# Optimization experiments

Measured on AMD Instinct MI355X. Metric: run time of the kernel, lower is better.

The kernel has to match this reference:

```python
import jax, jax.numpy as jnp
import numpy as np
import math

D_MODEL = 768
HEADS = 12
D_FF = 3072
B, S = 2, 2048


def layer_norm(x, g, b, eps=1e-6):
    mu = jnp.mean(x, axis=-1, keepdims=True)
    var = jnp.mean((x - mu) ** 2, axis=-1, keepdims=True)
    return (x - mu) / jnp.sqrt(var + eps) * g + b


def gelu_tanh(x):
    c = math.sqrt(2.0 / math.pi)
    return 0.5 * x * (1.0 + jnp.tanh(c * (x + 0.044715 * x ** 3)))


def setup_inputs() -> dict:
    key = jax.random.key(0)
    ks = jax.random.split(key, 12)
    s = 0.02
    inp = {
        "iter": 1,
        "query": jax.random.normal(ks[0], (B, S, D_MODEL), jnp.float32),
        "inputs": jax.random.normal(ks[1], (B, S, D_MODEL), jnp.float32),
        "mask": jax.random.randint(ks[2], (B, S), 0, 2).astype(bool),
        "Wq": jax.random.normal(ks[3], (D_MODEL, D_MODEL), jnp.float32) * s,
        "bq": jnp.zeros((D_MODEL,), jnp.float32),
        "Wk": jax.random.normal(ks[4], (D_MODEL, D_MODEL), jnp.float32) * s,
        "bk": jnp.zeros((D_MODEL,), jnp.float32),
        "Wv": jax.random.normal(ks[5], (D_MODEL, D_MODEL), jnp.float32) * s,
        "bv": jnp.zeros((D_MODEL,), jnp.float32),
        "Wo": jax.random.normal(ks[6], (D_MODEL, D_MODEL), jnp.float32) * s,
        "bo": jnp.zeros((D_MODEL,), jnp.float32),
        "ln1_g": jnp.ones((D_MODEL,), jnp.float32),
        "ln1_b": jnp.zeros((D_MODEL,), jnp.float32),
        "W1": jax.random.normal(ks[7], (D_MODEL, D_FF), jnp.float32) * s,
        "b1": jnp.zeros((D_FF,), jnp.float32),
        "W2": jax.random.normal(ks[8], (D_FF, D_MODEL), jnp.float32) * s,
        "b2": jnp.zeros((D_MODEL,), jnp.float32),
        "ln2_g": jnp.ones((D_MODEL,), jnp.float32),
        "ln2_b": jnp.zeros((D_MODEL,), jnp.float32),
    }
    return inp


def reference(iter, query, inputs, mask, Wq, bq, Wk, bk, Wv, bv, Wo, bo,
              ln1_g, ln1_b, W1, b1, W2, b2, ln2_g, ln2_b):
    dh = D_MODEL // HEADS
    # pre-LN (skipped when iter == 0)
    x = layer_norm(inputs, ln1_g, ln1_b) if iter != 0 else inputs
    # QKV projections -> [B, H, S, dh]
    def heads(t):
        return t.reshape(B, S, HEADS, dh).transpose(0, 2, 1, 3)
    q = heads(x @ Wq + bq) / math.sqrt(dh)
    k = heads(x @ Wk + bk)
    v = heads(x @ Wv + bv)
    scores = jnp.einsum("bhqd,bhkd->bhqk", q, k)
    scores = jnp.where(mask[:, None, None, :], -1e18, scores)
    attn = jax.nn.softmax(scores, axis=-1)
    ctx = jnp.einsum("bhqk,bhkd->bhqd", attn, v)
    ctx = ctx.transpose(0, 2, 1, 3).reshape(B, S, D_MODEL)
    attn_out = ctx @ Wo + bo
    out = attn_out + inputs  # dropout=0 -> identity
    # FFN with residual pre-LN and tanh-GELU
    h = layer_norm(out, ln2_g, ln2_b)
    inter = gelu_tanh(h @ W1 + b1)
    return inter @ W2 + b2 + out
```

## Files before the change

kernel.cpp:

```cpp
#include <hip/hip_runtime.h>
#include <hip/hip_bf16.h>
#include <stdint.h>

#define D_MODEL 768
#define HEADS   12
#define DHEAD   64
#define D_FF    3072
#define BB      2
#define SS      2048
#define MTOT    (BB*SS)

typedef uint16_t u16;
typedef uint32_t u32;
typedef __attribute__((ext_vector_type(8))) short short8;
typedef __attribute__((ext_vector_type(4))) short short4v;
typedef __attribute__((ext_vector_type(4))) float f32x4;
typedef __attribute__((ext_vector_type(16))) float f32x16;
typedef __attribute__((ext_vector_type(2))) unsigned uint2v;

__device__ __forceinline__ u16 f2bf(float f) {
    union { float f; u32 u; } v; v.f = f;
    u32 r = v.u + 0x7fffu + ((v.u >> 16) & 1u);
    return (u16)(r >> 16);
}

__device__ __forceinline__ float bf2f(u16 u) {
    union { u32 u; float f; } v; v.u = ((u32)u) << 16;
    return v.f;
}

__device__ __forceinline__ float exp2_fast(float x) {
#if __has_builtin(__builtin_amdgcn_exp2f)
    return __builtin_amdgcn_exp2f(x);
#else
    return exp2f(x);
#endif
}

__device__ __forceinline__ u32 cvtpk(float a, float b) {
    u32 r;
    asm("v_cvt_pk_bf16_f32 %0, %1, %2" : "=v"(r) : "v"(a), "v"(b));
    return r;
}

__device__ __forceinline__ void plswap(u32& a, u32& b, int hi) {
#if __has_builtin(__builtin_amdgcn_permlane32_swap)
    uint2v r = __builtin_amdgcn_permlane32_swap(a, b, false, false);
    a = r[0]; b = r[1];
#else
    u32 ax = (u32)__shfl_xor((int)a, 32), bx = (u32)__shfl_xor((int)b, 32);
    u32 na = hi ? bx : a, nb = hi ? b : ax;
    a = na; b = nb;
#endif
}

__device__ __forceinline__ void gload16(const void* g, void* l) {
    __builtin_amdgcn_global_load_lds(
        (const __attribute__((address_space(1))) u32*)g,
        (__attribute__((address_space(3))) u32*)l, 16, 0, 0);
}

#define MFMA16(a, b, c) __builtin_amdgcn_mfma_f32_16x16x32_bf16((a), (b), (c), 0, 0, 0)
#define MFMA32(a, b, c) __builtin_amdgcn_mfma_f32_32x32x16_bf16((a), (b), (c), 0, 0, 0)

__device__ __forceinline__ float gelu_tanh_f(float x) {
    float x3 = x * x * x;
    return 0.5f * x * (1.0f + tanhf(0.7978845608028654f * (x + 0.044715f * x3)));
}

__global__ __launch_bounds__(256)
void transpose_cast(const float* __restrict__ W, u16* __restrict__ Wt, int R, int C) {
    __shared__ float tile[32][33];
    int bx = blockIdx.x, by = blockIdx.y;
    int x = threadIdx.x & 31, y0 = threadIdx.x >> 5;
#pragma unroll
    for (int i = 0; i < 4; ++i) {
        int y = y0 + i * 8;
        tile[y][x] = W[(size_t)(by * 32 + y) * C + bx * 32 + x];
    }
    __syncthreads();
#pragma unroll
    for (int i = 0; i < 4; ++i) {
        int y = y0 + i * 8;
        Wt[(size_t)(bx * 32 + y) * R + by * 32 + x] = f2bf(tile[x][y]);
    }
}

__global__ __launch_bounds__(256)
void transpose_cast4(const float* __restrict__ W0, const float* __restrict__ W1,
                     const float* __restrict__ W2, const float* __restrict__ W3,
                     u16* __restrict__ T0, u16* __restrict__ T1,
                     u16* __restrict__ T2, u16* __restrict__ T3) {
    const int z = blockIdx.z;
    const float* W = z == 0 ? W0 : z == 1 ? W1 : z == 2 ? W2 : W3;
    u16*         T = z == 0 ? T0 : z == 1 ? T1 : z == 2 ? T2 : T3;
    __shared__ float tile[32][33];
    int bx = blockIdx.x, by = blockIdx.y;
    int x = threadIdx.x & 31, y0 = threadIdx.x >> 5;
#pragma unroll
    for (int i = 0; i < 4; ++i) {
        int y = y0 + i * 8;
        tile[y][x] = W[(size_t)(by * 32 + y) * 768 + bx * 32 + x];
    }
    __syncthreads();
#pragma unroll
    for (int i = 0; i < 4; ++i) {
        int y = y0 + i * 8;
        T[(size_t)(bx * 32 + y) * 768 + by * 32 + x] = f2bf(tile[x][y]);
    }
}

__global__ void maskprep(const int* __restrict__ m, float* __restrict__ vz,
                         u16* __restrict__ m01, int n) {
    int i = blockIdx.x * 256 + threadIdx.x;
    if (i < n) {
        float v = m[i] ? 0.0f : 1.0f;
        vz[i] = v;
        m01[i] = f2bf(v);
    }
}

__global__ __launch_bounds__(256)
void ln_bf16(const float* __restrict__ in, const float* __restrict__ g,
             const float* __restrict__ bta, u16* __restrict__ out,
             const int* __restrict__ iterp, int checkIter) {
    int row = blockIdx.x, tid = threadIdx.x;
    const float* x = in + (size_t)row * D_MODEL;
    float v0 = x[tid], v1 = x[tid + 256], v2 = x[tid + 512];
    float s = v0 + v1 + v2;
    float s2 = v0 * v0 + v1 * v1 + v2 * v2;
#pragma unroll
    for (int o = 1; o < 64; o <<= 1) { s += __shfl_xor(s, o); s2 += __shfl_xor(s2, o); }
    __shared__ float sh[8];
    int w = tid >> 6;
    if ((tid & 63) == 0) { sh[w] = s; sh[4 + w] = s2; }
    __syncthreads();
    s = sh[0] + sh[1] + sh[2] + sh[3];
    s2 = sh[4] + sh[5] + sh[6] + sh[7];
    float mu = s * (1.0f / 768.0f);
    float var = s2 * (1.0f / 768.0f) - mu * mu;
    float rstd = rsqrtf(var + 1e-6f);
    bool skip = checkIter && (iterp[0] == 0);
    u16* o0 = out + (size_t)row * D_MODEL;
    if (skip) {
        o0[tid] = f2bf(v0); o0[tid + 256] = f2bf(v1); o0[tid + 512] = f2bf(v2);
    } else {
        o0[tid]       = f2bf((v0 - mu) * rstd * g[tid]       + bta[tid]);
        o0[tid + 256] = f2bf((v1 - mu) * rstd * g[tid + 256] + bta[tid + 256]);
        o0[tid + 512] = f2bf((v2 - mu) * rstd * g[tid + 512] + bta[tid + 512]);
    }
}

__global__ __launch_bounds__(256)
void ln_fuse(const float* __restrict__ pf, const float* __restrict__ bias,
             const float* __restrict__ res, const float* __restrict__ g,
             const float* __restrict__ bta, float* __restrict__ outm,
             u16* __restrict__ out) {
    int row = blockIdx.x, tid = threadIdx.x;
    size_t i0 = (size_t)row * D_MODEL + tid;
    const float* pf1 = pf + (size_t)MTOT * D_MODEL;
    float v0 = pf[i0]       + pf1[i0]       + bias[tid]       + res[i0];
    float v1 = pf[i0 + 256] + pf1[i0 + 256] + bias[tid + 256] + res[i0 + 256];
    float v2 = pf[i0 + 512] + pf1[i0 + 512] + bias[tid + 512] + res[i0 + 512];
    outm[i0] = v0; outm[i0 + 256] = v1; outm[i0 + 512] = v2;
    float s = v0 + v1 + v2;
    float s2 = v0 * v0 + v1 * v1 + v2 * v2;
#pragma unroll
    for (int o = 1; o < 64; o <<= 1) { s += __shfl_xor(s, o); s2 += __shfl_xor(s2, o); }
    __shared__ float sh[8];
    int w = tid >> 6;
    if ((tid & 63) == 0) { sh[w] = s; sh[4 + w] = s2; }
    __syncthreads();
    s = sh[0] + sh[1] + sh[2] + sh[3];
    s2 = sh[4] + sh[5] + sh[6] + sh[7];
    float mu = s * (1.0f / 768.0f);
    float var = s2 * (1.0f / 768.0f) - mu * mu;
    float rstd = rsqrtf(var + 1e-6f);
    u16* o0 = out + (size_t)row * D_MODEL;
    o0[tid]       = f2bf((v0 - mu) * rstd * g[tid]       + bta[tid]);
    o0[tid + 256] = f2bf((v1 - mu) * rstd * g[tid + 256] + bta[tid + 256]);
    o0[tid + 512] = f2bf((v2 - mu) * rstd * g[tid + 512] + bta[tid + 512]);
}

template <int MODE>
__global__ __launch_bounds__(256, 3)
void gemm_bt(const u16* __restrict__ A, const u16* __restrict__ Bt,
             int K, int N,
             const float* __restrict__ bias0, const float* __restrict__ bias1,
             const float* __restrict__ bias2,
             const float* __restrict__ res,
             float* __restrict__ outF, u16* __restrict__ oq,
             u16* __restrict__ ok, u16* __restrict__ ov) {
    __shared__ __align__(16) u16 aT[3][128 * 32];
    __shared__ __align__(16) u16 bT[3][128 * 32];
    const int tid = threadIdx.x;
    const int lane = tid & 63;
    const int w = tid >> 6;
    const int wr = w >> 1, wc = w & 1;
    const int lm = lane & 15, lq = lane >> 4;
    const int bm = blockIdx.y, bn = blockIdx.x;
    const int kzlen = K / gridDim.z;
    const int kbeg = blockIdx.z * kzlen;
    const int nsteps = kzlen >> 5;

    const u16* Abase = A  + (size_t)(bm * 128) * K + kbeg;
    const u16* Bbase = Bt + (size_t)(bn * 128) * K + kbeg;

    auto stage = [&](int buf, int t) {
        int k0 = t * 32;
#pragma unroll
        for (int j = 0; j < 2; ++j) {
            int d = j * 256 + tid;
            int row = d >> 2, p = d & 3;
            int src = (p ^ (row & 3)) * 8;
            gload16(Abase + (size_t)row * K + k0 + src, aT[buf] + (j * 256 + w * 64) * 8);
            gload16(Bbase + (size_t)row * K + k0 + src, bT[buf] + (j * 256 + w * 64) * 8);
        }
    };

    f32x4 acc[4][4] = {};
    stage(0, 0);
    if (nsteps > 1) stage(1, 1);

#pragma unroll 1
    for (int t = 0; t < nsteps; ++t) {
        if (t + 1 < nsteps) asm volatile("s_waitcnt vmcnt(4)" ::: "memory");
        else                asm volatile("s_waitcnt vmcnt(0)" ::: "memory");
        __syncthreads();
        const u16* Ab = aT[t % 3];
        const u16* Bb = bT[t % 3];
        short8 av[4], bv[4];
#pragma unroll
        for (int m = 0; m < 4; ++m) {
            int row = wr * 64 + m * 16 + lm;
            av[m] = *(const short8*)(Ab + row * 32 + ((lq ^ (row & 3)) * 8));
        }
#pragma unroll
        for (int n = 0; n < 4; ++n) {
            int row = wc * 64 + n * 16 + lm;
            bv[n] = *(const short8*)(Bb + row * 32 + ((lq ^ (row & 3)) * 8));
        }
#pragma unroll
        for (int m = 0; m < 4; ++m)
#pragma unroll
            for (int n = 0; n < 4; ++n)
                acc[m][n] = MFMA16(av[m], bv[n], acc[m][n]);
        if (t + 2 < nsteps) stage((t + 2) % 3, t + 2);
    }

#pragma unroll
    for (int m = 0; m < 4; ++m) {
#pragma unroll
        for (int n = 0; n < 4; ++n) {
            int col = bn * 128 + wc * 64 + n * 16 + lm;
#pragma unroll
            for (int r = 0; r < 4; ++r) {
                int row = bm * 128 + wr * 64 + m * 16 + lq * 4 + r;
                float v = acc[m][n][r];
                if (MODE == 0) {
                    int proj = col / D_MODEL;
                    int d = col - proj * D_MODEL;
                    int hh = d >> 6, dhi = d & 63;
                    int bb = row >> 11, sIdx = row & 2047;
                    if (proj == 0) {
                        v = (v + bias0[d]) * 0.18033688011112042f;
                        oq[((size_t)(bb * HEADS + hh) * SS + sIdx) * DHEAD + dhi] = f2bf(v);
                    } else if (proj == 1) {
                        v = v + bias1[d];
                        ok[((size_t)(bb * HEADS + hh) * SS + sIdx) * DHEAD + dhi] = f2bf(v);
                    } else {
                        v = (v + bias2[d]) * res[row];
                        ov[((size_t)(bb * HEADS + hh) * DHEAD + dhi) * SS + sIdx] = f2bf(v);
                    }
                } else if (MODE == 1) {
                    if (gridDim.z > 1) {
                        outF[((size_t)blockIdx.z * MTOT + row) * N + col] = v;
                    } else {
                        size_t idx = (size_t)row * N + col;
                        outF[idx] = v + bias0[col] + res[idx];
                    }
                } else {
                    float t2 = v + bias0[col];
                    oq[(size_t)row * N + col] = f2bf(gelu_tanh_f(t2));
                }
            }
        }
    }
}

__global__ __launch_bounds__(256)
void reduce_ks2(const float* __restrict__ pf, const float* __restrict__ bias,
                const float* __restrict__ res, float* __restrict__ out, int N) {
    size_t i = ((size_t)blockIdx.x * 256 + threadIdx.x) * 4;
    f32x4 s0 = *(const f32x4*)(pf + i);
    f32x4 s1 = *(const f32x4*)(pf + (size_t)MTOT * N + i);
    int col = (int)(i % (size_t)N);
    f32x4 b = *(const f32x4*)(bias + col);
    f32x4 r = *(const f32x4*)(res + i);
    f32x4 o;
#pragma unroll
    for (int e = 0; e < 4; ++e) o[e] = s0[e] + s1[e] + b[e] + r[e];
    *(f32x4*)(out + i) = o;
}

template <int NCH>
__global__ __launch_bounds__(256, 3)
void attn_fwd6(const u16* __restrict__ q, const u16* __restrict__ k,
               const u16* __restrict__ vtg, const u16* __restrict__ m01g,
               u16* __restrict__ po, float* __restrict__ pml) {
    constexpr int KLEN = SS / NCH;
    constexpr int KT   = KLEN / 64;
    __shared__ __align__(16) u16 kls[3][64 * 64];
    __shared__ __align__(16) u16 vls[3][64 * 64];
    __shared__ __align__(16) u16 m01l[KLEN];

    const int tid = threadIdx.x, lane = tid & 63, w = tid >> 6;
    const int lm = lane & 31, hi = lane >> 5;
    const int head = blockIdx.y;
    const int qblk = blockIdx.x / NCH, chunk = blockIdx.x % NCH;
    const int q0 = qblk * 128;
    const int k0 = chunk * KLEN;

    const u16* qbase = q + (size_t)head * SS * DHEAD;
    const u16* kbase = k + (size_t)head * SS * DHEAD;
    const u16* vbase = vtg + (size_t)head * DHEAD * SS;
    const u16* m01row = m01g + (head / HEADS) * SS;

    short8 qf[4];
    const int qrow = q0 + w * 32 + lm;
#pragma unroll
    for (int c = 0; c < 4; ++c)
        qf[c] = *(const short8*)(qbase + (size_t)qrow * DHEAD + c * 16 + hi * 8);

    if (tid < KLEN / 8)
        gload16(m01row + k0 + (size_t)tid * 8, m01l + (size_t)(tid >> 6) * 64 * 8);

    auto stage = [&](int buf, int t) {
#pragma unroll
        for (int j = 0; j < 2; ++j) {
            int c = j * 256 + tid;
            int row = c >> 3, jj = c & 7;
            gload16(kbase + (size_t)(k0 + t * 64 + row) * DHEAD + ((jj ^ (row & 7)) * 8),
                    kls[buf] + (j * 256 + w * 64) * 8);
            gload16(vbase + (size_t)row * SS + k0 + t * 64 + ((jj ^ (row & 7)) * 8),
                    vls[buf] + (j * 256 + w * 64) * 8);
        }
    };
    stage(0, 0);
    if (KT > 1) stage(1, 1);

    f32x16 o0 = {}, o1 = {}, accl = {};

#pragma unroll 1
    for (int t = 0; t < KT; ++t) {
        if (t + 1 < KT) asm volatile("s_waitcnt vmcnt(4)" ::: "memory");
        else            asm volatile("s_waitcnt vmcnt(0)" ::: "memory");
        __syncthreads();
        const u16* kb = kls[t % 3];
        const u16* vb = vls[t % 3];
#pragma unroll
        for (int s = 0; s < 2; ++s) {
            short8 av[4];
#pragma unroll
            for (int c = 0; c < 4; ++c)
                av[c] = *(const short8*)(kb + (s * 32 + lm) * 64 + (((c * 2 + hi) ^ (lm & 7)) * 8));
            short8 vf[4];
#pragma unroll
            for (int kc = 0; kc < 2; ++kc)
#pragma unroll
                for (int df = 0; df < 2; ++df)
                    vf[kc * 2 + df] = *(const short8*)(vb + (df * 32 + lm) * 64 +
                                                       (((s * 4 + kc * 2 + hi) ^ (lm & 7)) * 8));
            short8 mf0 = *(const short8*)(m01l + t * 64 + s * 32 + hi * 8);
            short8 mf1 = *(const short8*)(m01l + t * 64 + s * 32 + 16 + hi * 8);

            f32x16 st = {};
#pragma unroll
            for (int c = 0; c < 4; ++c) st = MFMA32(av[c], qf[c], st);

            float p[16];
#pragma unroll
            for (int r = 0; r < 16; ++r) p[r] = exp2_fast(st[r]);

            u32 W[8];
#pragma unroll
            for (int t8 = 0; t8 < 8; ++t8) W[t8] = cvtpk(p[2 * t8], p[2 * t8 + 1]);
            union { u32 wd[4]; short8 s8; } pf0, pf1;
            u32 a0w = W[0], b0w = W[2]; plswap(a0w, b0w, hi);
            u32 a1w = W[1], b1w = W[3]; plswap(a1w, b1w, hi);
            u32 a2w = W[4], b2w = W[6]; plswap(a2w, b2w, hi);
            u32 a3w = W[5], b3w = W[7]; plswap(a3w, b3w, hi);
            pf0.wd[0] = a0w; pf0.wd[1] = a1w; pf0.wd[2] = b0w; pf0.wd[3] = b1w;
            pf1.wd[0] = a2w; pf1.wd[1] = a3w; pf1.wd[2] = b2w; pf1.wd[3] = b3w;

            accl = MFMA32(mf0, pf0.s8, accl);
            accl = MFMA32(mf1, pf1.s8, accl);
            o0 = MFMA32(vf[0], pf0.s8, o0);
            o1 = MFMA32(vf[1], pf0.s8, o1);
            o0 = MFMA32(vf[2], pf1.s8, o0);
            o1 = MFMA32(vf[3], pf1.s8, o1);
        }
        if (t + 2 < KT) stage((t + 2) % 3, t + 2);
    }

    const int pc = (head * 16 + qblk) * NCH + chunk;
    u16* orow = po + ((size_t)pc * 128 + (w * 32 + lm)) * 64;
#pragma unroll
    for (int g = 0; g < 4; ++g) {
        short4v pk0, pk1;
#pragma unroll
        for (int e = 0; e < 4; ++e) {
            pk0[e] = (short)f2bf(o0[g * 4 + e]);
            pk1[e] = (short)f2bf(o1[g * 4 + e]);
        }
        *(short4v*)(orow + g * 8 + hi * 4) = pk0;
        *(short4v*)(orow + 32 + g * 8 + hi * 4) = pk1;
    }
    if (hi == 0)
        pml[(size_t)pc * 128 + (w * 32 + lm)] = accl[0];
}

__global__ __launch_bounds__(256)
void attn_merge(const u16* __restrict__ po, const float* __restrict__ pml,
                u16* __restrict__ ctx, int nch) {
    const int head = blockIdx.y;
    const int bb = head / HEADS, hh = head % HEADS;
    const int rl = threadIdx.x >> 4, dg = threadIdx.x & 15;
    const int s = blockIdx.x * 16 + rl;
    const int qb = s >> 7, qr = s & 127;
    const int pcb = (head * 16 + qb) * nch;

    float denom = 0.0f;
    float acc[4] = {0.0f, 0.0f, 0.0f, 0.0f};
#pragma unroll 4
    for (int c = 0; c < nch; ++c) {
        denom += pml[((size_t)(pcb + c)) * 128 + qr];
        const u16* op = po + (((size_t)(pcb + c) * 128 + qr) * 64) + dg * 4;
        short4v a = *(const short4v*)op;
#pragma unroll
        for (int e = 0; e < 4; ++e) acc[e] += bf2f((u16)a[e]);
    }
    float inv = 1.0f / denom;
    short4v r;
#pragma unroll
    for (int e = 0; e < 4; ++e) r[e] = (short)f2bf(acc[e] * inv);
    *(short4v*)(ctx + ((size_t)(bb * SS + s)) * D_MODEL + hh * DHEAD + dg * 4) = r;
}

extern "C" void kernel_launch(void* const* d_in, const int* in_sizes, int n_in,
                              void* d_out, int out_size, void* d_ws, size_t ws_size,
                              hipStream_t stream) {
    const int*   iterp  = (const int*)  d_in[0];
    const float* inputs = (const float*)d_in[2];
    const int*   mask   = (const int*)  d_in[3];
    const float* Wq = (const float*)d_in[4];
    const float* bq = (const float*)d_in[5];
    const float* Wk = (const float*)d_in[6];
    const float* bk = (const float*)d_in[7];
    const float* Wv = (const float*)d_in[8];
    const float* bv = (const float*)d_in[9];
    const float* Wo = (const float*)d_in[10];
    const float* bo = (const float*)d_in[11];
    const float* ln1g = (const float*)d_in[12];
    const float* ln1b = (const float*)d_in[13];
    const float* W1 = (const float*)d_in[14];
    const float* b1 = (const float*)d_in[15];
    const float* W2 = (const float*)d_in[16];
    const float* b2 = (const float*)d_in[17];
    const float* ln2g = (const float*)d_in[18];
    const float* ln2b = (const float*)d_in[19];
    float* outp = (float*)d_out;

    char* ws = (char*)d_ws;
    size_t off = 0;
    auto alloc = [&](size_t bytes) -> void* {
        void* p = ws + off;
        off += (bytes + 255) & ~(size_t)255;
        return p;
    };
    u16*   wqkv_t = (u16*)  alloc((size_t)2304 * 768 * 2);
    u16*   wo_t   = (u16*)  alloc((size_t)768 * 768 * 2);
    u16*   w1_t   = (u16*)  alloc((size_t)3072 * 768 * 2);
    u16*   w2_t   = (u16*)  alloc((size_t)768 * 3072 * 2);
    float* vzf    = (float*)alloc((size_t)MTOT * 4);
    u16*   m01    = (u16*)  alloc((size_t)MTOT * 2);
    u16*   xh     = (u16*)  alloc((size_t)MTOT * 768 * 2);
    u16*   qb     = (u16*)  alloc((size_t)MTOT * 768 * 2);
    u16*   kbuf   = (u16*)  alloc((size_t)MTOT * 768 * 2);
    u16*   vtb    = (u16*)  alloc((size_t)MTOT * 768 * 2);
    u16*   ctxb   = (u16*)  alloc((size_t)MTOT * 768 * 2);
    float* outm   = (float*)alloc((size_t)MTOT * 768 * 4);
    u16*   inter  = qb;

    float* pfbuf = (float*)alloc((size_t)2 * MTOT * 768 * 4);
    const bool split_ok = (off <= ws_size);

    float* pml = (float*)xh;

    dim3 blk(256);
    transpose_cast4<<<dim3(24, 24, 4), blk, 0, stream>>>(
        Wq, Wk, Wv, Wo,
        wqkv_t, wqkv_t + 768 * 768, wqkv_t + 2 * 768 * 768, wo_t);
    transpose_cast<<<dim3(96, 24), blk, 0, stream>>>(W1, w1_t, 768, 3072);
    transpose_cast<<<dim3(24, 96), blk, 0, stream>>>(W2, w2_t, 3072, 768);
    maskprep<<<dim3(16), blk, 0, stream>>>(mask, vzf, m01, MTOT);

    ln_bf16<<<dim3(MTOT), blk, 0, stream>>>(inputs, ln1g, ln1b, xh, iterp, 1);

    gemm_bt<0><<<dim3(2304 / 128, MTOT / 128), blk, 0, stream>>>(
        xh, wqkv_t, 768, 2304, bq, bk, bv, vzf, nullptr, qb, kbuf, vtb);

    if (split_ok) {
        u16* po = (u16*)pfbuf;
        attn_fwd6<4><<<dim3(16 * 4, BB * HEADS), blk, 0, stream>>>(
            qb, kbuf, vtb, m01, po, pml);
        attn_merge<<<dim3(SS / 16, BB * HEADS), blk, 0, stream>>>(po, pml, ctxb, 4);
    } else {
        u16* po = (u16*)outm;
        attn_fwd6<2><<<dim3(16 * 2, BB * HEADS), blk, 0, stream>>>(
            qb, kbuf, vtb, m01, po, pml);
        attn_merge<<<dim3(SS / 16, BB * HEADS), blk, 0, stream>>>(po, pml, ctxb, 2);
    }

    if (split_ok) {
        gemm_bt<1><<<dim3(768 / 128, MTOT / 128, 2), blk, 0, stream>>>(
            ctxb, wo_t, 768, 768, nullptr, nullptr, nullptr, nullptr,
            pfbuf, nullptr, nullptr, nullptr);
        ln_fuse<<<dim3(MTOT), blk, 0, stream>>>(pfbuf, bo, inputs, ln2g, ln2b, outm, xh);
    } else {
        gemm_bt<1><<<dim3(768 / 128, MTOT / 128), blk, 0, stream>>>(
            ctxb, wo_t, 768, 768, bo, nullptr, nullptr, inputs, outm, nullptr, nullptr, nullptr);
        ln_bf16<<<dim3(MTOT), blk, 0, stream>>>(outm, ln2g, ln2b, xh, iterp, 0);
    }

    gemm_bt<2><<<dim3(3072 / 128, MTOT / 128), blk, 0, stream>>>(
        xh, w1_t, 768, 3072, b1, nullptr, nullptr, nullptr, nullptr, inter, nullptr, nullptr);

    if (split_ok) {
        gemm_bt<1><<<dim3(768 / 128, MTOT / 128, 2), blk, 0, stream>>>(
            inter, w2_t, 3072, 768, nullptr, nullptr, nullptr, nullptr,
            pfbuf, nullptr, nullptr, nullptr);
        reduce_ks2<<<dim3(MTOT * 768 / 1024), blk, 0, stream>>>(pfbuf, b2, outm, outp, 768);
    } else {
        gemm_bt<1><<<dim3(768 / 128, MTOT / 128), blk, 0, stream>>>(
            inter, w2_t, 3072, 768, b2, nullptr, nullptr, outm, outp, nullptr, nullptr, nullptr);
    }
}
```

Measured before the change: 221.5 us.

## Split-K the fused QKV projection GEMM with a separate bf16 partial-reduce kernel

The QKV projection GEMM now splits K in two along grid z, doubling the block count. Each half writes bf16 partial sums into a scratch buffer. A new reduce_qkv kernel adds the two halves and applies the biases, the Q scaling and the V mask. It then scatters into the head-major Q/K layout and, through a shared-memory tile, into the transposed V layout. This aims to improve CU occupancy and load balance on the GEMM, at the cost of an extra launch, extra global traffic for the partials and extra rounding from storing partials in bf16.

New measurement: 218.6 us (median of 3 runs). Within noise of the previous version (-1.3%).

```diff
diff --git a/kernel.cpp b/kernel.cpp
--- a/kernel.cpp
+++ b/kernel.cpp
@@ -279,12 +279,78 @@
                         size_t idx = (size_t)row * N + col;
                         outF[idx] = v + bias0[col] + res[idx];
                     }
-                } else {
+                } else if (MODE == 2) {
                     float t2 = v + bias0[col];
                     oq[(size_t)row * N + col] = f2bf(gelu_tanh_f(t2));
+                } else {
+                    oq[((size_t)blockIdx.z * MTOT + row) * N + col] = f2bf(v);
                 }
             }
         }
+    }
+}
+
+__global__ __launch_bounds__(256)
+void reduce_qkv(const u16* __restrict__ P,
+                const float* __restrict__ bq, const float* __restrict__ bk,
+                const float* __restrict__ bv, const float* __restrict__ vz,
+                u16* __restrict__ qq, u16* __restrict__ kk,
+                u16* __restrict__ vt) {
+    const int zone = blockIdx.y;
+    const int tid = threadIdx.x;
+    const u16* P1 = P + (size_t)MTOT * 2304;
+
+    if (zone < 2) {
+        int idx = blockIdx.x * 256 + tid;
+        int row = idx / 96;
+        int c8  = idx - row * 96;
+        int col = zone * 768 + c8 * 8;
+        short8 a = *(const short8*)(P  + (size_t)row * 2304 + col);
+        short8 b = *(const short8*)(P1 + (size_t)row * 2304 + col);
+        const float* bias = zone ? bk : bq;
+        union { u16 u[8]; short8 s; } o;
+#pragma unroll
+        for (int e = 0; e < 8; ++e) {
+            float v = bf2f((u16)a[e]) + bf2f((u16)b[e]) + bias[c8 * 8 + e];
+            if (zone == 0) v *= 0.18033688011112042f;
+            o.u[e] = f2bf(v);
+        }
+        int d = c8 * 8, hh = d >> 6, dhi = d & 63;
+        int bb = row >> 11, s = row & 2047;
+        u16* dst = (zone ? kk : qq) +
+                   ((size_t)(bb * HEADS + hh) * SS + s) * DHEAD + dhi;
+        *(short8*)dst = o.s;
+    } else {
+        if (blockIdx.x >= 768) return;
+        __shared__ u16 tile[64][72];
+        int tr = blockIdx.x / 12, tc = blockIdx.x - tr * 12;
+        int r0 = tr * 64;
+#pragma unroll
+        for (int p = 0; p < 2; ++p) {
+            int lr = p * 32 + (tid >> 3);
+            int coff = (tid & 7) * 8;
+            int row = r0 + lr;
+            const u16* p0 = P + (size_t)row * 2304 + 1536 + tc * 64 + coff;
+            short8 a = *(const short8*)p0;
+            short8 b = *(const short8*)(p0 + (size_t)MTOT * 2304);
+            float zf = vz[row];
+#pragma unroll
+            for (int e = 0; e < 8; ++e) {
+                float v = (bf2f((u16)a[e]) + bf2f((u16)b[e]) +
+                           bv[tc * 64 + coff + e]) * zf;
+                tile[lr][coff + e] = f2bf(v);
+            }
+        }
+        __syncthreads();
+        int c = tid >> 2, sg = tid & 3;
+        union { u16 u[16]; f32x4 v4[4]; } buf;
+#pragma unroll
+        for (int i = 0; i < 16; ++i) buf.u[i] = tile[sg * 16 + i][c];
+        int bb = r0 >> 11;
+        int s0 = (r0 & 2047) + sg * 16;
+        u16* dst = vt + ((size_t)(bb * HEADS + tc) * DHEAD + c) * SS + s0;
+        *(f32x4*)dst = buf.v4[0];
+        *(f32x4*)(dst + 8) = buf.v4[1];
     }
 }
 
@@ -507,8 +573,17 @@
 
     ln_bf16<<<dim3(MTOT), blk, 0, stream>>>(inputs, ln1g, ln1b, xh, iterp, 1);
 
-    gemm_bt<0><<<dim3(2304 / 128, MTOT / 128), blk, 0, stream>>>(
-        xh, wqkv_t, 768, 2304, bq, bk, bv, vzf, nullptr, qb, kbuf, vtb);
+    if (split_ok) {
+        u16* P = (u16*)outm;
+        gemm_bt<3><<<dim3(2304 / 128, MTOT / 128, 2), blk, 0, stream>>>(
+            xh, wqkv_t, 768, 2304, nullptr, nullptr, nullptr, nullptr,
+            nullptr, P, nullptr, nullptr);
+        reduce_qkv<<<dim3(1536, 3), blk, 0, stream>>>(
+            P, bq, bk, bv, vzf, qb, kbuf, vtb);
+    } else {
+        gemm_bt<0><<<dim3(2304 / 128, MTOT / 128), blk, 0, stream>>>(
+            xh, wqkv_t, 768, 2304, bq, bk, bv, vzf, nullptr, qb, kbuf, vtb);
+    }
 
     if (split_ok) {
         u16* po = (u16*)pfbuf;
```
